# Kernel tuning notes

Hardware: AMD Instinct MI355X
Metric: run time of the kernel (lower is better)

The kernel has to match this reference:

```python
import jax, jax.numpy as jnp
import numpy as np

N, M, A, O, F = 4, 64, 64, 5, 256


def _sph_harm_l2(R):
    # real spherical harmonics up to l=2 (9 components) of the unit direction
    r = jnp.linalg.norm(R, axis=-1, keepdims=True)
    u = R / (r + 1e-12)
    x, y, z = u[..., 0], u[..., 1], u[..., 2]
    c1 = 0.4886025119029199
    c2 = 1.0925484305920792
    return jnp.stack([
        jnp.full_like(x, 0.28209479177387814),
        c1 * y, c1 * z, c1 * x,
        c2 * x * y, c2 * y * z,
        0.31539156525252005 * (3.0 * z * z - 1.0),
        c2 * x * z,
        0.5462742152960396 * (x * x - y * y),
    ], axis=-1)  # [..., 9]


def setup_inputs() -> dict:
    key = jax.random.key(0)
    ks = jax.random.split(key, 6)
    return {
        "ao_embeddings": jax.random.normal(ks[0], (N, M, A, O, F), jnp.float32),
        "C": jax.random.normal(ks[1], (N, M, A, O), jnp.float32),
        "S": jax.random.normal(ks[2], (N, A, 3, A, 3), jnp.float32),
        "R": jax.random.normal(ks[3], (N, M, A, 3), jnp.float32),
        "w_stack": jax.random.normal(ks[4], (5, 3, 3), jnp.float32) * 0.5,
        "cgc": jax.random.normal(ks[5], (9, 9, 9), jnp.float32) * 0.1,
    }


def reference(ao_embeddings, C, S, R, w_stack, cgc):
    # mo_features: [n, m, a, o=5, f]
    mo = C[..., None] * ao_embeddings
    # 5-step bilinear transform of the overlap-like tensor S [n, a, 3, b, 3]
    Sc = S
    for i in range(5):
        w = w_stack[i]  # [3, 3]
        Sc = jnp.einsum('ab,cd,kibjd->kiajc', w, w, Sc)
        Sc = jax.nn.swish(Sc)
    filt = jnp.array([[1., 1., 0.], [1., 1., 0.], [0., 0., 1.]], Sc.dtype)
    Sc = filt[None, None, :, None, :] * Sc
    idx = jnp.array([0, 1, 2, 2, 2])  # tf.repeat(repeats=[1, 1, 3]) -> size 5
    Sc = jnp.take(jnp.take(Sc, idx, axis=2), idx, axis=4)  # [n, a, 5, b, 5]
    # message passing over atom pairs: [n, m, b, p=5, f]
    mo = jnp.einsum('nmaof,naobp->nmbpf', mo, Sc)
    # unsorted_segment_sum with segment_ids [0,0,1,2,3] into 9 slots == matmul with one-hot map
    seg = jnp.zeros((5, 9), mo.dtype).at[jnp.arange(5), jnp.array([0, 0, 1, 2, 3])].set(1.0)
    mo = jnp.einsum('nmbpf,pq->nmbqf', mo, seg)  # [n, m, a, 9, f]
    # coupling: sph harmonics * ||C|| (tf.repeat over f == broadcast, folded into einsum)
    Cn = jnp.linalg.norm(C, axis=-1)            # [n, m, a]
    coup = _sph_harm_l2(R) * Cn[..., None]      # [n, m, a, 9]
    # CG contraction + sum over atoms a: [n, m, i=9, f]
    out = jnp.einsum('nmapf,nmak,kip->nmif', mo, coup, cgc)
    return jnp.transpose(out, (0, 1, 3, 2))     # [n, m, f, 9]
```

## Files before the change

kernel.cpp:

```cpp
#include <hip/hip_runtime.h>
#include <math.h>


__global__ void k_sc(const float* __restrict__ S, const float* __restrict__ wst,
                     float* __restrict__ G) {
    int t = blockIdx.x * 128 + threadIdx.x;
    int n = t >> 12;
    int a = (t >> 6) & 63;
    int b = t & 63;
    float M[3][3];
#pragma unroll
    for (int x = 0; x < 3; ++x)
#pragma unroll
        for (int y = 0; y < 3; ++y)
            M[x][y] = S[(((n * 64 + a) * 3 + x) * 64 + b) * 3 + y];
#pragma unroll
    for (int it = 0; it < 5; ++it) {
        float w[3][3];
#pragma unroll
        for (int x = 0; x < 3; ++x)
#pragma unroll
            for (int y = 0; y < 3; ++y)
                w[x][y] = wst[it * 9 + x * 3 + y];
        float T[3][3];
#pragma unroll
        for (int x = 0; x < 3; ++x)
#pragma unroll
            for (int d = 0; d < 3; ++d)
                T[x][d] = w[x][0] * M[0][d] + w[x][1] * M[1][d] + w[x][2] * M[2][d];
#pragma unroll
        for (int x = 0; x < 3; ++x)
#pragma unroll
            for (int c = 0; c < 3; ++c) {
                float v = T[x][0] * w[c][0] + T[x][1] * w[c][1] + T[x][2] * w[c][2];
                M[x][c] = v / (1.f + expf(-v));
            }
    }
    float g0 = M[0][0] + M[0][1];
    float g1 = M[1][0] + M[1][1];
    float gz = M[2][2];
    size_t base = (size_t)n * 12288 + (size_t)b * 64 + a;
    G[base]          = g0;
    G[base + 4096]   = g1;
    G[base + 8192]   = gz;
}

__global__ __launch_bounds__(576) void k_w3(
        const float* __restrict__ C, const float* __restrict__ R,
        const float* __restrict__ cgc, const float* __restrict__ G,
        float* __restrict__ coeff) {
    __shared__ float s_coup[64 * 9];
    __shared__ float s_D[2 * 9 * 64];
    __shared__ float s_W3[64 * 3 * 9];

    const int nm = blockIdx.x;
    const int n = nm >> 6;
    const int tid = threadIdx.x;

    if (tid < 64) {
        const int b = tid;
        const float* rp = R + ((size_t)nm * 64 + b) * 3;
        float x = rp[0], y = rp[1], z = rp[2];
        float rn = sqrtf(x * x + y * y + z * z) + 1e-12f;
        x /= rn; y /= rn; z /= rn;
        const float* cp = C + ((size_t)nm * 64 + b) * 5;
        float cn = 0.f;
#pragma unroll
        for (int o = 0; o < 5; ++o) cn += cp[o] * cp[o];
        cn = sqrtf(cn);
        const float c1 = 0.4886025119029199f;
        const float c2 = 1.0925484305920792f;
        float Y[9];
        Y[0] = 0.28209479177387814f;
        Y[1] = c1 * y;
        Y[2] = c1 * z;
        Y[3] = c1 * x;
        Y[4] = c2 * x * y;
        Y[5] = c2 * y * z;
        Y[6] = 0.31539156525252005f * (3.f * z * z - 1.f);
        Y[7] = c2 * x * z;
        Y[8] = 0.5462742152960396f * (x * x - y * y);
#pragma unroll
        for (int k = 0; k < 9; ++k) s_coup[b * 9 + k] = Y[k] * cn;
    }
    __syncthreads();

    {
        const int b = tid & 63, i = tid >> 6;
        float d0 = 0.f, dz = 0.f;
#pragma unroll
        for (int k = 0; k < 9; ++k) {
            float cp = s_coup[b * 9 + k];
            const float* cg = cgc + k * 81 + i * 9;
            d0 = fmaf(cp, cg[0], d0);
            dz = fmaf(cp, cg[1] + cg[2] + cg[3], dz);
        }
        s_D[(0 * 9 + i) * 64 + b] = d0;
        s_D[(1 * 9 + i) * 64 + b] = dz;
    }
    __syncthreads();

    const int pp = __builtin_amdgcn_readfirstlane(tid >> 6);
    const int lane = tid & 63;
    {
        const int u = pp / 3;
        const int i0 = (pp % 3) * 3;
        const int pm = (u == 2) ? 1 : 0;
        const float* gp = G + (size_t)n * 12288 + (size_t)u * 4096 + lane;
        const float* dp = &s_D[(pm * 9 + i0) * 64];
        float a0 = 0.f, a1 = 0.f, a2 = 0.f;
#pragma unroll 8
        for (int b = 0; b < 64; ++b) {
            float g = gp[b * 64];
            a0 = fmaf(g, dp[b], a0);
            a1 = fmaf(g, dp[64 + b], a1);
            a2 = fmaf(g, dp[128 + b], a2);
        }
        s_W3[(lane * 3 + u) * 9 + i0 + 0] = a0;
        s_W3[(lane * 3 + u) * 9 + i0 + 1] = a1;
        s_W3[(lane * 3 + u) * 9 + i0 + 2] = a2;
    }
    __syncthreads();

    const float* Cb = C + (size_t)nm * 320;
    float* cf = coeff + (size_t)nm * 320 * 9;
    for (int e = tid; e < 2880; e += 576) {
        int a = e / 45;
        int rem = e - a * 45;
        int o = rem / 9;
        int i = rem - o * 9;
        int u = o < 2 ? o : 2;
        cf[e] = Cb[a * 5 + o] * s_W3[(a * 3 + u) * 9 + i];
    }
}

__global__ __launch_bounds__(512) void k_out(
        const float* __restrict__ ao, const float* __restrict__ coeff,
        float* __restrict__ out) {
    __shared__ float s_par[8][128 * 9];
    const int bid = blockIdx.x;
    const int nm = bid >> 1;
    const int fh = bid & 1;
    const int tid = threadIdx.x;
    const int lane = tid & 63;
    const int w = __builtin_amdgcn_readfirstlane(tid >> 6);
    const int rbase = w * 40;
    const float* ap = ao + ((size_t)nm * 320 + rbase) * 256 + fh * 128 + lane * 2;
    const float* cf = coeff + ((size_t)nm * 320 + rbase) * 9;
    float acc[9][2];
#pragma unroll
    for (int i = 0; i < 9; ++i) { acc[i][0] = 0.f; acc[i][1] = 0.f; }
#pragma unroll 8
    for (int r = 0; r < 40; ++r) {
        float2 v = *reinterpret_cast<const float2*>(ap + (size_t)r * 256);
#pragma unroll
        for (int i = 0; i < 9; ++i) {
            float c = cf[r * 9 + i];
            acc[i][0] = fmaf(c, v.x, acc[i][0]);
            acc[i][1] = fmaf(c, v.y, acc[i][1]);
        }
    }
#pragma unroll
    for (int j = 0; j < 2; ++j)
#pragma unroll
        for (int i = 0; i < 9; ++i)
            s_par[w][(lane * 2 + j) * 9 + i] = acc[i][j];
    __syncthreads();
    for (int s = tid; s < 1152; s += 512) {
        float sum = 0.f;
#pragma unroll
        for (int w2 = 0; w2 < 8; ++w2) sum += s_par[w2][s];
        out[(size_t)nm * 2304 + fh * 1152 + s] = sum;
    }
}

extern "C" void kernel_launch(void* const* d_in, const int* in_sizes, int n_in,
                              void* d_out, int out_size, void* d_ws, size_t ws_size,
                              hipStream_t stream) {
    (void)in_sizes; (void)n_in; (void)out_size; (void)ws_size;
    const float* ao  = (const float*)d_in[0];
    const float* C   = (const float*)d_in[1];
    const float* S   = (const float*)d_in[2];
    const float* R   = (const float*)d_in[3];
    const float* wst = (const float*)d_in[4];
    const float* cgc = (const float*)d_in[5];
    float* out = (float*)d_out;
    float* ws = (float*)d_ws;
    float* G     = ws;
    float* coeff = ws + 49152;

    hipLaunchKernelGGL(k_sc,  dim3(128), dim3(128), 0, stream, S, wst, G);
    hipLaunchKernelGGL(k_w3,  dim3(256), dim3(576), 0, stream, C, R, cgc, G, coeff);
    hipLaunchKernelGGL(k_out, dim3(512), dim3(512), 0, stream, ao, coeff, out);
}
```

Baseline: 33.67 us.

## Fold C scaling into output kernel and reduce atoms via wave shuffles

```diff
diff --git a/kernel.cpp b/kernel.cpp
--- a/kernel.cpp
+++ b/kernel.cpp
@@ -1,6 +1,9 @@
 #include <hip/hip_runtime.h>
 #include <math.h>
 
+
+typedef float v4f __attribute__((ext_vector_type(4)));
+static __device__ inline v4f splat4(float s) { return (v4f){s, s, s, s}; }
 
 __global__ void k_sc(const float* __restrict__ S, const float* __restrict__ wst,
                      float* __restrict__ G) {
@@ -48,10 +51,10 @@
 __global__ __launch_bounds__(576) void k_w3(
         const float* __restrict__ C, const float* __restrict__ R,
         const float* __restrict__ cgc, const float* __restrict__ G,
-        float* __restrict__ coeff) {
+        float* __restrict__ wsW3) {
     __shared__ float s_coup[64 * 9];
     __shared__ float s_D[2 * 9 * 64];
-    __shared__ float s_W3[64 * 3 * 9];
+    __shared__ float s_W3[64 * 27];
 
     const int nm = blockIdx.x;
     const int n = nm >> 6;
@@ -116,61 +119,86 @@
             a1 = fmaf(g, dp[64 + b], a1);
             a2 = fmaf(g, dp[128 + b], a2);
         }
-        s_W3[(lane * 3 + u) * 9 + i0 + 0] = a0;
-        s_W3[(lane * 3 + u) * 9 + i0 + 1] = a1;
-        s_W3[(lane * 3 + u) * 9 + i0 + 2] = a2;
-    }
-    __syncthreads();
-
-    const float* Cb = C + (size_t)nm * 320;
-    float* cf = coeff + (size_t)nm * 320 * 9;
-    for (int e = tid; e < 2880; e += 576) {
-        int a = e / 45;
-        int rem = e - a * 45;
-        int o = rem / 9;
-        int i = rem - o * 9;
-        int u = o < 2 ? o : 2;
-        cf[e] = Cb[a * 5 + o] * s_W3[(a * 3 + u) * 9 + i];
+        s_W3[lane * 27 + u * 9 + i0 + 0] = a0;
+        s_W3[lane * 27 + u * 9 + i0 + 1] = a1;
+        s_W3[lane * 27 + u * 9 + i0 + 2] = a2;
+    }
+    __syncthreads();
+
+    float* wp = wsW3 + (size_t)nm * 1792;
+    for (int e = tid; e < 1792; e += 576) {
+        int a = e / 28, q = e - a * 28;
+        wp[e] = (q < 27) ? s_W3[a * 27 + q] : 0.f;
     }
 }
 
 __global__ __launch_bounds__(512) void k_out(
-        const float* __restrict__ ao, const float* __restrict__ coeff,
-        float* __restrict__ out) {
-    __shared__ float s_par[8][128 * 9];
-    const int bid = blockIdx.x;
-    const int nm = bid >> 1;
-    const int fh = bid & 1;
+        const float* __restrict__ ao, const float* __restrict__ C,
+        const float* __restrict__ wsW3, float* __restrict__ out) {
+    __shared__ float s_W3[64 * 28];
+    __shared__ float s_C[320];
+    const int nm = blockIdx.x;
     const int tid = threadIdx.x;
+    {
+        const float* wp = wsW3 + (size_t)nm * 1792;
+        for (int e = tid; e < 1792; e += 512) s_W3[e] = wp[e];
+        const float* cp = C + (size_t)nm * 320;
+        for (int e = tid; e < 320; e += 512) s_C[e] = cp[e];
+    }
+    __syncthreads();
+
+    const int w = tid >> 6;
     const int lane = tid & 63;
-    const int w = __builtin_amdgcn_readfirstlane(tid >> 6);
-    const int rbase = w * 40;
-    const float* ap = ao + ((size_t)nm * 320 + rbase) * 256 + fh * 128 + lane * 2;
-    const float* cf = coeff + ((size_t)nm * 320 + rbase) * 9;
-    float acc[9][2];
-#pragma unroll
-    for (int i = 0; i < 9; ++i) { acc[i][0] = 0.f; acc[i][1] = 0.f; }
-#pragma unroll 8
-    for (int r = 0; r < 40; ++r) {
-        float2 v = *reinterpret_cast<const float2*>(ap + (size_t)r * 256);
+    const int fgrp = lane & 7;
+    const int agrp = lane >> 3;
+    const int f0 = w * 32 + fgrp * 4;
+    const float* ap = ao + (size_t)nm * 81920 + (size_t)agrp * 1280 + f0;
+
+    v4f acc[9];
+#pragma unroll
+    for (int i = 0; i < 9; ++i) acc[i] = splat4(0.f);
+
+#pragma unroll
+    for (int t = 0; t < 8; ++t) {
+        const int a = agrp + 8 * t;
+        const float* aop = ap + t * 10240;
+        v4f v0 = *(const v4f*)(aop + 0 * 256);
+        v4f v1 = *(const v4f*)(aop + 1 * 256);
+        v4f v2 = *(const v4f*)(aop + 2 * 256);
+        v4f v3 = *(const v4f*)(aop + 3 * 256);
+        v4f v4 = *(const v4f*)(aop + 4 * 256);
+        const float* cc = &s_C[a * 5];
+        v4f e0 = splat4(cc[0]) * v0;
+        v4f e1 = splat4(cc[1]) * v1;
+        v4f e2 = splat4(cc[2]) * v2 + splat4(cc[3]) * v3 + splat4(cc[4]) * v4;
+        const float* w3 = &s_W3[a * 28];
+#pragma unroll
+        for (int i = 0; i < 9; ++i)
+            acc[i] += splat4(w3[i]) * e0 + splat4(w3[9 + i]) * e1 + splat4(w3[18 + i]) * e2;
+    }
+
+#pragma unroll
+    for (int mask = 8; mask <= 32; mask <<= 1) {
 #pragma unroll
         for (int i = 0; i < 9; ++i) {
-            float c = cf[r * 9 + i];
-            acc[i][0] = fmaf(c, v.x, acc[i][0]);
-            acc[i][1] = fmaf(c, v.y, acc[i][1]);
+#pragma unroll
+            for (int j = 0; j < 4; ++j)
+                acc[i][j] += __shfl_xor(acc[i][j], mask, 64);
         }
     }
-#pragma unroll
-    for (int j = 0; j < 2; ++j)
-#pragma unroll
-        for (int i = 0; i < 9; ++i)
-            s_par[w][(lane * 2 + j) * 9 + i] = acc[i][j];
-    __syncthreads();
-    for (int s = tid; s < 1152; s += 512) {
-        float sum = 0.f;
-#pragma unroll
-        for (int w2 = 0; w2 < 8; ++w2) sum += s_par[w2][s];
-        out[(size_t)nm * 2304 + fh * 1152 + s] = sum;
+
+    if (agrp == 0) {
+        v4f buf4[9];
+        float* bp = (float*)buf4;
+#pragma unroll
+        for (int j = 0; j < 4; ++j)
+#pragma unroll
+            for (int i = 0; i < 9; ++i)
+                bp[j * 9 + i] = acc[i][j];
+        float* op = out + (size_t)nm * 2304 + (size_t)f0 * 9;
+#pragma unroll
+        for (int q = 0; q < 9; ++q)
+            *(v4f*)(op + q * 4) = buf4[q];
     }
 }
 
@@ -186,10 +214,10 @@
     const float* cgc = (const float*)d_in[5];
     float* out = (float*)d_out;
     float* ws = (float*)d_ws;
-    float* G     = ws;
-    float* coeff = ws + 49152;
+    float* G    = ws;
+    float* wsW3 = ws + 49152;
 
     hipLaunchKernelGGL(k_sc,  dim3(128), dim3(128), 0, stream, S, wst, G);
-    hipLaunchKernelGGL(k_w3,  dim3(256), dim3(576), 0, stream, C, R, cgc, G, coeff);
-    hipLaunchKernelGGL(k_out, dim3(512), dim3(512), 0, stream, ao, coeff, out);
-}
+    hipLaunchKernelGGL(k_w3,  dim3(256), dim3(576), 0, stream, C, R, cgc, G, wsW3);
+    hipLaunchKernelGGL(k_out, dim3(256), dim3(512), 0, stream, ao, C, wsW3, out);
+}
```

Result: faster. 31.57 us (-6.2%).
